# Kernel optimization log

Hardware: AMD Instinct MI355X
Metric: run time of the kernel (lower is better)

Reference implementation:

```python
import jax, jax.numpy as jnp
import numpy as np

B, T, D, H, N, S, FF = 8, 1024, 512, 8, 256, 256, 2048
AUD, TXT = 768, 256  # audio_input_dim, text_feature_dim (hardcoded in module)
EPS = 1e-5


def _ln(x, g, b):
    m = x.mean(-1, keepdims=True)
    v = ((x - m) ** 2).mean(-1, keepdims=True)
    return (x - m) / jnp.sqrt(v + EPS) * g + b


def _lin(x, w, b):
    return x @ w + b


def setup_inputs() -> dict:
    keys = iter(jax.random.split(jax.random.key(0), 64))
    def rn(shape, s=0.02):
        return jax.random.normal(next(keys), shape, jnp.float32) * s
    inp = {
        'x': jax.random.normal(next(keys), (B, T, D), jnp.float32),
        'xf': jax.random.normal(next(keys), (B, AUD), jnp.float32),
        'xw': jax.random.normal(next(keys), (B, N, TXT), jnp.float32),
        'xs': jax.random.normal(next(keys), (B, S, D), jnp.float32),
        # feat_proj (linear variant)
        'fp_w': rn((D, D)), 'fp_b': rn((D,)),
        # self-attention
        'sa_ng': 1.0 + rn((D,)), 'sa_nb': rn((D,)),
        'sa_qw': rn((D, D)), 'sa_qb': rn((D,)),
        'sa_kw': rn((D, D)), 'sa_kb': rn((D,)),
        'sa_vw': rn((D, D)), 'sa_vb': rn((D,)),
        'sa_ow': rn((D, D)), 'sa_ob': rn((D,)),
        # cross-attention
        'ca_ng': 1.0 + rn((D,)), 'ca_nb': rn((D,)),
        'ca_tng': 1.0 + rn((D,)), 'ca_tnb': rn((D,)),
        'ca_sng': 1.0 + rn((D,)), 'ca_snb': rn((D,)),
        'ca_qw': rn((D, D)), 'ca_qb': rn((D,)),
        'ca_kw': rn((D, D)), 'ca_kb': rn((D,)),
        'ca_vw': rn((D, D)), 'ca_vb': rn((D,)),
        'ca_apw': rn((AUD, TXT)), 'ca_apb': rn((TXT,)),
        'ca_atw': rn((TXT, D)), 'ca_atb': rn((D,)),
        'ca_ow': rn((D, D)), 'ca_ob': rn((D,)),
        'an_g': 1.0 + rn((D,)), 'an_b': rn((D,)),
        # FFN
        'ffn_w1': rn((D, FF)), 'ffn_b1': rn((FF,)),
        'ffn_w2': rn((FF, D)), 'ffn_b2': rn((D,)),
        'ffn_ng': 1.0 + rn((D,)), 'ffn_nb': rn((D,)),
        'ffn_ow': rn((D, D)), 'ffn_ob': rn((D,)),
    }
    return inp


def reference(x, xf, xw, xs, fp_w, fp_b, sa_ng, sa_nb, sa_qw, sa_qb, sa_kw, sa_kb,
              sa_vw, sa_vb, sa_ow, sa_ob, ca_ng, ca_nb, ca_tng, ca_tnb, ca_sng, ca_snb,
              ca_qw, ca_qb, ca_kw, ca_kb, ca_vw, ca_vb, ca_apw, ca_apb, ca_atw, ca_atb,
              ca_ow, ca_ob, an_g, an_b, ffn_w1, ffn_b1, ffn_w2, ffn_b2, ffn_ng, ffn_nb,
              ffn_ow, ffn_ob):
    Bx, Tx, Dx = x.shape
    dh = Dx // H
    # feat_proj + detached residual (x_ori = x.detach().clone())
    xp = _lin(x, fp_w, fp_b) + jax.lax.stop_gradient(x)

    # ---- self-attention block ----
    xn = _ln(xp, sa_ng, sa_nb)
    q = _lin(xn, sa_qw, sa_qb).reshape(Bx, Tx, H, dh)
    k = _lin(xn, sa_kw, sa_kb).reshape(Bx, Tx, H, dh)
    v = _lin(xn, sa_vw, sa_vb).reshape(Bx, Tx, H, dh)
    scores = jnp.einsum('bthd,bshd->bths', q, k) / jnp.sqrt(jnp.float32(dh))
    ao = jnp.einsum('bths,bshd->bthd', jax.nn.softmax(scores, -1), v).reshape(Bx, Tx, Dx)
    sa_out = xp + _lin(jax.nn.silu(ao), sa_ow, sa_ob)
    y1 = _ln(sa_out + xp, an_g, an_b)

    # ---- cross-attention block (linear attention over text/audio + semantic) ----
    Nw = xw.shape[1]
    xf_p = _lin(xf, ca_apw, ca_apb)                              # [B, 256]
    xf_e = jnp.broadcast_to(xf_p[:, None, :], (Bx, Nw, TXT))
    xw_xf = _lin(jnp.concatenate([xw, xf_e], axis=1), ca_atw, ca_atb)  # [B, 2N, D]
    tn = _ln(xw_xf, ca_tng, ca_tnb)
    sn = _ln(xs, ca_sng, ca_snb)
    cq = jax.nn.softmax(_lin(_ln(y1, ca_ng, ca_nb), ca_qw, ca_qb).reshape(Bx, Tx, H, dh), -1)
    ck = jax.nn.softmax(_lin(tn, ca_kw, ca_kb).reshape(Bx, 2 * Nw, H, dh), 1)
    sk = jax.nn.softmax(_lin(sn, ca_kw, ca_kb).reshape(Bx, -1, H, dh), 1)
    cv = _lin(tn, ca_vw, ca_vb).reshape(Bx, 2 * Nw, H, dh)
    sv = _lin(sn, ca_vw, ca_vb).reshape(Bx, -1, H, dh)
    att = jnp.einsum('bnhd,bnhl->bhdl', ck, cv)                  # [B,H,dh,dh]
    satt = jnp.einsum('bshd,bshl->bhsl', sk, sv)                 # [B,H,S,dh]
    cy = jnp.einsum('bthd,bhdl->bthl', cq, att).reshape(Bx, Tx, Dx)
    sy = jnp.einsum('bthd,bhsl->bthl', cq, satt).reshape(Bx, Tx, Dx)
    ca_out = y1 + _lin(jax.nn.silu(cy + sy), ca_ow, ca_ob)
    y2 = _ln(ca_out + y1, an_g, an_b)

    # ---- FFN block ----
    h = jax.nn.gelu(_lin(y2, ffn_w1, ffn_b1), approximate=False)
    h = _ln(_lin(h, ffn_w2, ffn_b2), ffn_ng, ffn_nb)
    ffn_out = y2 + _lin(jax.nn.silu(h), ffn_ow, ffn_ob)
    y3 = _ln(ffn_out + y2, an_g, an_b)
    return y3
```

## Files before the change

### kernel.cpp

```cpp
#include <hip/hip_runtime.h>
#include <math.h>

typedef unsigned short u16;
typedef short s16x8 __attribute__((ext_vector_type(8)));
typedef float f32x4 __attribute__((ext_vector_type(4)));
typedef unsigned short u16x8 __attribute__((ext_vector_type(8)));
typedef unsigned short u16x4 __attribute__((ext_vector_type(4)));

#define DD 512

__device__ __forceinline__ float silu_f(float x) { return x / (1.f + __expf(-x)); }
__device__ __forceinline__ float gelu_f(float x) {
  float y = 1.5957691216f * (x + 0.044715f * x * x * x);
  return x / (1.f + __expf(-y));
}
__device__ __forceinline__ u16 f2bf(float f) {
  unsigned u = __float_as_uint(f);
  return (u16)((u + 0x7fffu + ((u >> 16) & 1u)) >> 16);
}
__device__ __forceinline__ float bf2f(u16 u) { return __uint_as_float(((unsigned)u) << 16); }
__device__ __forceinline__ unsigned cvtpk_bf16(float a, float b) {
  unsigned r;
  asm("v_cvt_pk_bf16_f32 %0, %1, %2" : "=v"(r) : "v"(a), "v"(b));
  return r;
}

__device__ __forceinline__ void gload16(const void* g, void* l) {
  __builtin_amdgcn_global_load_lds(
      (const __attribute__((address_space(1))) void*)(g),
      (__attribute__((address_space(3))) void*)(l), 16, 0, 0);
}

template<int ACT, int OB>
__global__ __launch_bounds__(256) void gemm64(
    const u16* __restrict__ A, const u16* __restrict__ Bt,
    const float* __restrict__ bias, const float* __restrict__ res, float res_scale,
    float* __restrict__ outf, float* __restrict__ outf2,
    u16* __restrict__ outb, u16* __restrict__ outb2,
    int M, int N, int K)
{
  __shared__ u16 As[2][4096];
  __shared__ u16 Bs[2][4096];
  const int t = threadIdx.x, l = t & 63, w = t >> 6;
  const int gx = gridDim.x;
  const int nblk = gx * gridDim.y;
  const int id = blockIdx.y * gx + blockIdx.x;
  const int nid = (id & 7) * (nblk >> 3) + (id >> 3);
  const int bm = (nid / gx) << 6, bn = (nid % gx) << 6;
  const int wr = (w >> 1) << 5, wc = (w & 1) << 5;
  f32x4 acc[2][2];
#pragma unroll
  for (int i = 0; i < 2; ++i)
#pragma unroll
    for (int j = 0; j < 2; ++j) acc[i][j] = (f32x4){0.f, 0.f, 0.f, 0.f};

  auto stage = [&](int k0, int buf) {
#pragma unroll
    for (int i = 0; i < 2; ++i) {
      int c = t + (i << 8);
      int row = c >> 3, cq = c & 7;
      int cs = cq ^ (row & 7);
      gload16(A + (size_t)(bm + row) * K + k0 + cs * 8, (char*)As[buf] + (i << 12) + (w << 10));
      gload16(Bt + (size_t)(bn + row) * K + k0 + cs * 8, (char*)Bs[buf] + (i << 12) + (w << 10));
    }
  };
  stage(0, 0);
  asm volatile("s_waitcnt vmcnt(0)" ::: "memory");
  __builtin_amdgcn_s_barrier();

  const int fr = l & 15, q0 = l >> 4;
  const int nk = K >> 6;
  int cur = 0;
  for (int kt = 0; kt < nk; ++kt) {
    if (kt + 1 < nk) stage((kt + 1) << 6, cur ^ 1);
    s16x8 af[2][2], bg[2][2];
#pragma unroll
    for (int kk = 0; kk < 2; ++kk)
#pragma unroll
      for (int i = 0; i < 2; ++i) {
        int ra = wr + i * 16 + fr;
        af[kk][i] = *(const s16x8*)&As[cur][ra * 64 + (((q0 + kk * 4)) ^ (ra & 7)) * 8];
        int rb = wc + i * 16 + fr;
        bg[kk][i] = *(const s16x8*)&Bs[cur][rb * 64 + (((q0 + kk * 4)) ^ (rb & 7)) * 8];
      }
    asm volatile("s_waitcnt lgkmcnt(0)" ::: "memory");
    __builtin_amdgcn_sched_barrier(0);
#pragma unroll
    for (int kk = 0; kk < 2; ++kk)
#pragma unroll
      for (int mi = 0; mi < 2; ++mi)
#pragma unroll
        for (int ni = 0; ni < 2; ++ni)
          acc[mi][ni] = __builtin_amdgcn_mfma_f32_16x16x32_bf16(af[kk][mi], bg[kk][ni], acc[mi][ni], 0, 0, 0);
    asm volatile("s_waitcnt vmcnt(0)" ::: "memory");
    __builtin_amdgcn_s_barrier();
    cur ^= 1;
  }

  const int cr0 = (l >> 4) << 2, cc = l & 15;

  if (OB == 0 || OB == 4) {
    float* fdst = outf;
    int coff = bn, ld = N;
    if (OB == 4) { ld = 512; coff = bn & 511; if (bn >= 512) fdst = outf2; }
#pragma unroll
    for (int ni = 0; ni < 2; ++ni) {
      int n = bn + wc + ni * 16 + cc;
      int col = coff + wc + ni * 16 + cc;
      float bia = bias[n];
#pragma unroll
      for (int mi = 0; mi < 2; ++mi) {
#pragma unroll
        for (int r = 0; r < 4; ++r) {
          int m = bm + wr + mi * 16 + cr0 + r;
          size_t off = (size_t)m * ld + col;
          float o = acc[mi][ni][r] + bia;
          if (ACT == 1) o = gelu_f(o);
          if (res) o = fmaf(res_scale, res[off], o);
          fdst[off] = o;
        }
      }
    }
  } else if (OB == 1 || OB == 5) {
#pragma unroll
    for (int ni = 0; ni < 2; ++ni) {
      int n = bn + wc + ni * 16 + cc;
      float bia = bias[n];
#pragma unroll
      for (int mi = 0; mi < 2; ++mi) {
#pragma unroll
        for (int r = 0; r < 4; ++r) {
          int m = bm + wr + mi * 16 + cr0 + r;
          size_t off = (size_t)m * N + n;
          float o = acc[mi][ni][r] + bia;
          if (ACT == 1) o = gelu_f(o);
          if (OB == 5) o = fmaf(res_scale, res[off], o);
          outb[off] = f2bf(o);
        }
      }
    }
  } else if (OB == 6) {
    float* smem = (float*)&As[0][0];
    float ev[2][2][4];
    float part[2][4];
#pragma unroll
    for (int mi = 0; mi < 2; ++mi)
#pragma unroll
      for (int r = 0; r < 4; ++r) part[mi][r] = 0.f;
#pragma unroll
    for (int ni = 0; ni < 2; ++ni) {
      float bia = bias[bn + wc + ni * 16 + cc];
#pragma unroll
      for (int mi = 0; mi < 2; ++mi)
#pragma unroll
        for (int r = 0; r < 4; ++r) {
          float e = __expf(acc[mi][ni][r] + bia);
          ev[mi][ni][r] = e;
          part[mi][r] += e;
        }
    }
#pragma unroll
    for (int mi = 0; mi < 2; ++mi)
#pragma unroll
      for (int r = 0; r < 4; ++r) {
        float s = part[mi][r];
        s += __shfl_xor(s, 1); s += __shfl_xor(s, 2);
        s += __shfl_xor(s, 4); s += __shfl_xor(s, 8);
        part[mi][r] = s;
      }
    __syncthreads();
#pragma unroll
    for (int mi = 0; mi < 2; ++mi)
#pragma unroll
      for (int r = 0; r < 4; ++r) {
        int trow = wr + mi * 16 + cr0 + r;
        smem[(w & 1) * 64 + trow] = part[mi][r];
      }
    __syncthreads();
#pragma unroll
    for (int mi = 0; mi < 2; ++mi)
#pragma unroll
      for (int r = 0; r < 4; ++r) {
        int trow = wr + mi * 16 + cr0 + r;
        float inv = 1.f / (smem[trow] + smem[64 + trow]);
#pragma unroll
        for (int ni = 0; ni < 2; ++ni) {
          int n = bn + wc + ni * 16 + cc;
          outf[(size_t)(bm + trow) * 512 + n] = ev[mi][ni][r] * inv;
        }
      }
  } else {
    int seg = bn >> 9;
    int colbase = bn & 511;
    if (seg < 2) {
      u16* dst = seg ? outb2 : outb;
#pragma unroll
      for (int ni = 0; ni < 2; ++ni) {
        int col = colbase + wc + ni * 16 + cc;
        float bia = bias[bn + wc + ni * 16 + cc];
#pragma unroll
        for (int mi = 0; mi < 2; ++mi) {
#pragma unroll
          for (int r = 0; r < 4; ++r) {
            int m = bm + wr + mi * 16 + cr0 + r;
            dst[(size_t)m * 512 + col] = f2bf(acc[mi][ni][r] + bia);
          }
        }
      }
    } else {
      u16* tile = &As[0][0];
      __syncthreads();
#pragma unroll
      for (int ni = 0; ni < 2; ++ni) {
        int lc = wc + ni * 16 + cc;
        float bia = bias[bn + wc + ni * 16 + cc];
#pragma unroll
        for (int mi = 0; mi < 2; ++mi) {
          int lm0 = wr + mi * 16 + cr0;
          u16x4 pk;
#pragma unroll
          for (int r = 0; r < 4; ++r) pk[r] = f2bf(acc[mi][ni][r] + bia);
          *(u16x4*)&tile[lc * 64 + (lm0 ^ ((lc & 7) << 3))] = pk;
        }
      }
      __syncthreads();
      int h = colbase >> 6;
      size_t vrow0 = ((size_t)((bm >> 10) * 8 + h)) * 64;
      int d = t >> 3, c8 = (t & 7) << 3;
      *(u16x8*)(((u16*)outf) + (vrow0 + d) * 1024 + (bm & 1023) + c8) =
          *(u16x8*)&tile[d * 64 + (c8 ^ ((d & 7) << 3))];
    }
  }
}

template<int ACT, int OBF>
__global__ __launch_bounds__(512) void gemm8w(
    const u16* __restrict__ A, const u16* __restrict__ Bt,
    const float* __restrict__ bias, float* __restrict__ outf, u16* __restrict__ outb,
    int M, int N, int K)
{
  __shared__ u16 As[2][4096];
  __shared__ u16 Bs[2][8192];
  const int t = threadIdx.x, l = t & 63, w = t >> 6;
  const int gx = gridDim.x;
  const int nblk = gx * gridDim.y;
  const int id = blockIdx.y * gx + blockIdx.x;
  const int nid = (id & 7) * (nblk >> 3) + (id >> 3);
  const int bm = (nid / gx) << 7, bn = (nid % gx) << 8;
  const int wr = (w >> 2) << 6, wc = (w & 3) << 6;
  f32x4 acc[4][4];
#pragma unroll
  for (int i = 0; i < 4; ++i)
#pragma unroll
    for (int j = 0; j < 4; ++j) acc[i][j] = (f32x4){0.f, 0.f, 0.f, 0.f};

  auto stage = [&](int k0, int buf) {
    {
      int row = t >> 2, cq = t & 3;
      int cs = cq ^ ((row >> 1) & 3);
      gload16(A + (size_t)(bm + row) * K + k0 + cs * 8, (char*)As[buf] + (w << 10));
    }
#pragma unroll
    for (int i = 0; i < 2; ++i) {
      int c = t + (i << 9);
      int row = c >> 2, cq = c & 3;
      int cs = cq ^ ((row >> 1) & 3);
      gload16(Bt + (size_t)(bn + row) * K + k0 + cs * 8, (char*)Bs[buf] + ((w + (i << 3)) << 10));
    }
  };
  stage(0, 0);
  asm volatile("s_waitcnt vmcnt(0)" ::: "memory");
  __builtin_amdgcn_s_barrier();

  const int fr = l & 15, q0 = l >> 4;
  const int nk = K >> 5;
  int cur = 0;
  for (int kt = 0; kt < nk; ++kt) {
    if (kt + 1 < nk) stage((kt + 1) << 5, cur ^ 1);
    s16x8 af[4], bg[4];
#pragma unroll
    for (int i = 0; i < 4; ++i) {
      int ra = wr + i * 16 + fr;
      af[i] = *(const s16x8*)&As[cur][ra * 32 + (q0 ^ ((ra >> 1) & 3)) * 8];
      int rb = wc + i * 16 + fr;
      bg[i] = *(const s16x8*)&Bs[cur][rb * 32 + (q0 ^ ((rb >> 1) & 3)) * 8];
    }
    asm volatile("s_waitcnt lgkmcnt(0)" ::: "memory");
    __builtin_amdgcn_sched_barrier(0);
#pragma unroll
    for (int mi = 0; mi < 4; ++mi)
#pragma unroll
      for (int ni = 0; ni < 4; ++ni)
        acc[mi][ni] = __builtin_amdgcn_mfma_f32_16x16x32_bf16(af[mi], bg[ni], acc[mi][ni], 0, 0, 0);
    asm volatile("s_waitcnt vmcnt(0)" ::: "memory");
    __builtin_amdgcn_s_barrier();
    cur ^= 1;
  }

  const int cr0 = (l >> 4) << 2, cc = l & 15;
#pragma unroll
  for (int ni = 0; ni < 4; ++ni) {
    int n = bn + wc + ni * 16 + cc;
    float bia = bias[n];
#pragma unroll
    for (int mi = 0; mi < 4; ++mi) {
#pragma unroll
      for (int r = 0; r < 4; ++r) {
        int m = bm + wr + mi * 16 + cr0 + r;
        size_t off = (size_t)m * N + n;
        float o = acc[mi][ni][r] + bia;
        if (ACT == 1) o = gelu_f(o);
        if (OBF) outb[off] = f2bf(o);
        else outf[off] = o;
      }
    }
  }
}

__global__ __launch_bounds__(256) void xfp_k(
    const float* __restrict__ xf, const u16* __restrict__ apwT,
    const float* __restrict__ bias, float* __restrict__ xfp)
{
  int wid = blockIdx.x * 4 + (threadIdx.x >> 6);
  int lane = threadIdx.x & 63;
  int b = wid >> 8, n = wid & 255;
  const u16* wp = apwT + (size_t)n * 768;
  const float* xp = xf + (size_t)b * 768;
  float s = 0.f;
#pragma unroll
  for (int j = 0; j < 12; ++j) s = fmaf(xp[lane + j * 64], bf2f(wp[lane + j * 64]), s);
#pragma unroll
  for (int m = 1; m < 64; m <<= 1) s += __shfl_xor(s, m);
  if (lane == 0) xfp[wid] = s + bias[n];
}

__global__ __launch_bounds__(256) void biascat_k(
    const float* __restrict__ qb, const float* __restrict__ kb, const float* __restrict__ vb,
    const float* __restrict__ ckb, const float* __restrict__ cvb,
    float* __restrict__ bQKV, float* __restrict__ bKV)
{
  int t = blockIdx.x * 256 + threadIdx.x;
  if (t < 512) bQKV[t] = qb[t];
  else if (t < 1024) bQKV[t] = kb[t - 512];
  else if (t < 1536) bQKV[t] = vb[t - 1024];
  else if (t < 2048) bKV[t - 1536] = ckb[t - 1536];
  else if (t < 2560) bKV[t - 1536] = cvb[t - 2048];
}

__global__ __launch_bounds__(256) void ln_k(
    const float* __restrict__ src, const float* __restrict__ g,
    const float* __restrict__ b, float* __restrict__ out32, u16* __restrict__ out16,
    int rows, int do_silu)
{
  int lane = threadIdx.x & 63, wv = threadIdx.x >> 6;
  int row = (blockIdx.x << 2) + wv;
  if (row >= rows) return;
  const float* p = src + (size_t)row * DD;
  float4 v0 = *(const float4*)(p + lane * 4);
  float4 v1 = *(const float4*)(p + 256 + lane * 4);
  float s = v0.x + v0.y + v0.z + v0.w + v1.x + v1.y + v1.z + v1.w;
  float ss = v0.x*v0.x + v0.y*v0.y + v0.z*v0.z + v0.w*v0.w
           + v1.x*v1.x + v1.y*v1.y + v1.z*v1.z + v1.w*v1.w;
#pragma unroll
  for (int m = 1; m < 64; m <<= 1) { s += __shfl_xor(s, m); ss += __shfl_xor(ss, m); }
  float mean = s * (1.f / 512.f);
  float var = ss * (1.f / 512.f) - mean * mean;
  float rstd = rsqrtf(var + 1e-5f);
  float4 g0 = *(const float4*)(g + lane * 4);
  float4 g1 = *(const float4*)(g + 256 + lane * 4);
  float4 b0 = *(const float4*)(b + lane * 4);
  float4 b1 = *(const float4*)(b + 256 + lane * 4);
  float o[8];
  o[0] = (v0.x - mean) * rstd * g0.x + b0.x;
  o[1] = (v0.y - mean) * rstd * g0.y + b0.y;
  o[2] = (v0.z - mean) * rstd * g0.z + b0.z;
  o[3] = (v0.w - mean) * rstd * g0.w + b0.w;
  o[4] = (v1.x - mean) * rstd * g1.x + b1.x;
  o[5] = (v1.y - mean) * rstd * g1.y + b1.y;
  o[6] = (v1.z - mean) * rstd * g1.z + b1.z;
  o[7] = (v1.w - mean) * rstd * g1.w + b1.w;
  if (do_silu) {
#pragma unroll
    for (int j = 0; j < 8; ++j) o[j] = silu_f(o[j]);
  }
  if (out32) {
    *(float4*)(out32 + (size_t)row * DD + lane * 4) = make_float4(o[0], o[1], o[2], o[3]);
    *(float4*)(out32 + (size_t)row * DD + 256 + lane * 4) = make_float4(o[4], o[5], o[6], o[7]);
  }
  if (out16) {
    u16x4 h0, h1;
#pragma unroll
    for (int j = 0; j < 4; ++j) { h0[j] = f2bf(o[j]); h1[j] = f2bf(o[4 + j]); }
    *(u16x4*)(out16 + (size_t)row * DD + lane * 4) = h0;
    *(u16x4*)(out16 + (size_t)row * DD + 256 + lane * 4) = h1;
  }
}

__global__ __launch_bounds__(256) void lnb_k(
    const u16* __restrict__ src, const float* __restrict__ g,
    const float* __restrict__ b, float* __restrict__ out32, u16* __restrict__ out16,
    int rows, int do_silu)
{
  int lane = threadIdx.x & 63, wv = threadIdx.x >> 6;
  int row = (blockIdx.x << 2) + wv;
  if (row >= rows) return;
  const u16* p = src + (size_t)row * DD;
  u16x4 a0 = *(const u16x4*)(p + lane * 4);
  u16x4 a1 = *(const u16x4*)(p + 256 + lane * 4);
  float v[8];
#pragma unroll
  for (int j = 0; j < 4; ++j) { v[j] = bf2f(a0[j]); v[4 + j] = bf2f(a1[j]); }
  float s = 0.f, ss = 0.f;
#pragma unroll
  for (int j = 0; j < 8; ++j) { s += v[j]; ss = fmaf(v[j], v[j], ss); }
#pragma unroll
  for (int m = 1; m < 64; m <<= 1) { s += __shfl_xor(s, m); ss += __shfl_xor(ss, m); }
  float mean = s * (1.f / 512.f);
  float var = ss * (1.f / 512.f) - mean * mean;
  float rstd = rsqrtf(var + 1e-5f);
  float4 g0 = *(const float4*)(g + lane * 4);
  float4 g1 = *(const float4*)(g + 256 + lane * 4);
  float4 b0 = *(const float4*)(b + lane * 4);
  float4 b1 = *(const float4*)(b + 256 + lane * 4);
  float o[8];
  o[0] = (v[0] - mean) * rstd * g0.x + b0.x;
  o[1] = (v[1] - mean) * rstd * g0.y + b0.y;
  o[2] = (v[2] - mean) * rstd * g0.z + b0.z;
  o[3] = (v[3] - mean) * rstd * g0.w + b0.w;
  o[4] = (v[4] - mean) * rstd * g1.x + b1.x;
  o[5] = (v[5] - mean) * rstd * g1.y + b1.y;
  o[6] = (v[6] - mean) * rstd * g1.z + b1.z;
  o[7] = (v[7] - mean) * rstd * g1.w + b1.w;
  if (do_silu) {
#pragma unroll
    for (int j = 0; j < 8; ++j) o[j] = silu_f(o[j]);
  }
  if (out32) {
    *(float4*)(out32 + (size_t)row * DD + lane * 4) = make_float4(o[0], o[1], o[2], o[3]);
    *(float4*)(out32 + (size_t)row * DD + 256 + lane * 4) = make_float4(o[4], o[5], o[6], o[7]);
  }
  if (out16) {
    u16x4 h0, h1;
#pragma unroll
    for (int j = 0; j < 4; ++j) { h0[j] = f2bf(o[j]); h1[j] = f2bf(o[4 + j]); }
    *(u16x4*)(out16 + (size_t)row * DD + lane * 4) = h0;
    *(u16x4*)(out16 + (size_t)row * DD + 256 + lane * 4) = h1;
  }
}

__global__ __launch_bounds__(256) void ln2_k(
    const u16* __restrict__ src, const float* __restrict__ g1, const float* __restrict__ b1,
    const float* __restrict__ g2, const float* __restrict__ b2,
    float* __restrict__ out1, u16* __restrict__ out2, int rows)
{
  int lane = threadIdx.x & 63, wv = threadIdx.x >> 6;
  int row = (blockIdx.x << 2) + wv;
  if (row >= rows) return;
  const u16* p = src + (size_t)row * DD;
  u16x4 a0 = *(const u16x4*)(p + lane * 4);
  u16x4 a1 = *(const u16x4*)(p + 256 + lane * 4);
  float v[8];
#pragma unroll
  for (int j = 0; j < 4; ++j) { v[j] = bf2f(a0[j]); v[4 + j] = bf2f(a1[j]); }
  float s = 0.f, ss = 0.f;
#pragma unroll
  for (int j = 0; j < 8; ++j) { s += v[j]; ss = fmaf(v[j], v[j], ss); }
#pragma unroll
  for (int m = 1; m < 64; m <<= 1) { s += __shfl_xor(s, m); ss += __shfl_xor(ss, m); }
  float mean = s * (1.f / 512.f);
  float rstd = rsqrtf(ss * (1.f / 512.f) - mean * mean + 1e-5f);
  float4 G0 = *(const float4*)(g1 + lane * 4);
  float4 G1 = *(const float4*)(g1 + 256 + lane * 4);
  float4 B0 = *(const float4*)(b1 + lane * 4);
  float4 B1 = *(const float4*)(b1 + 256 + lane * 4);
  float y[8];
  y[0] = (v[0] - mean) * rstd * G0.x + B0.x;
  y[1] = (v[1] - mean) * rstd * G0.y + B0.y;
  y[2] = (v[2] - mean) * rstd * G0.z + B0.z;
  y[3] = (v[3] - mean) * rstd * G0.w + B0.w;
  y[4] = (v[4] - mean) * rstd * G1.x + B1.x;
  y[5] = (v[5] - mean) * rstd * G1.y + B1.y;
  y[6] = (v[6] - mean) * rstd * G1.z + B1.z;
  y[7] = (v[7] - mean) * rstd * G1.w + B1.w;
  *(float4*)(out1 + (size_t)row * DD + lane * 4) = make_float4(y[0], y[1], y[2], y[3]);
  *(float4*)(out1 + (size_t)row * DD + 256 + lane * 4) = make_float4(y[4], y[5], y[6], y[7]);
  float s2 = 0.f, ss2 = 0.f;
#pragma unroll
  for (int j = 0; j < 8; ++j) { s2 += y[j]; ss2 = fmaf(y[j], y[j], ss2); }
#pragma unroll
  for (int m = 1; m < 64; m <<= 1) { s2 += __shfl_xor(s2, m); ss2 += __shfl_xor(ss2, m); }
  float m2 = s2 * (1.f / 512.f);
  float r2 = rsqrtf(ss2 * (1.f / 512.f) - m2 * m2 + 1e-5f);
  float4 H0 = *(const float4*)(g2 + lane * 4);
  float4 H1 = *(const float4*)(g2 + 256 + lane * 4);
  float4 C0 = *(const float4*)(b2 + lane * 4);
  float4 C1 = *(const float4*)(b2 + 256 + lane * 4);
  u16x4 h0, h1;
  h0[0] = f2bf((y[0] - m2) * r2 * H0.x + C0.x);
  h0[1] = f2bf((y[1] - m2) * r2 * H0.y + C0.y);
  h0[2] = f2bf((y[2] - m2) * r2 * H0.z + C0.z);
  h0[3] = f2bf((y[3] - m2) * r2 * H0.w + C0.w);
  h1[0] = f2bf((y[4] - m2) * r2 * H1.x + C1.x);
  h1[1] = f2bf((y[5] - m2) * r2 * H1.y + C1.y);
  h1[2] = f2bf((y[6] - m2) * r2 * H1.z + C1.z);
  h1[3] = f2bf((y[7] - m2) * r2 * H1.w + C1.w);
  *(u16x4*)(out2 + (size_t)row * DD + lane * 4) = h0;
  *(u16x4*)(out2 + (size_t)row * DD + 256 + lane * 4) = h1;
}

__global__ __launch_bounds__(256) void attn3_k(
    const u16* __restrict__ q, const u16* __restrict__ k,
    const u16* __restrict__ vt, u16* __restrict__ out)
{
  __shared__ __align__(16) char KVb[2][2][8192];
  __shared__ __align__(16) char QP[16384];
  __shared__ float Lr[4][32];

  const int t = threadIdx.x, l = t & 63, w = t >> 6;
  const int id = blockIdx.x;
  const int blk = (id & 7) * 64 + (id >> 3);
  const int qt = blk & 7, h = (blk >> 3) & 7, b = blk >> 6;
  const size_t qbase = ((size_t)(b * 1024 + qt * 128)) * 512 + h * 64;
  const size_t kbase = ((size_t)(b * 1024)) * 512 + h * 64;
  const size_t vbase = ((size_t)((b * 8 + h) * 64)) * 1024;

#pragma unroll
  for (int i = 0; i < 4; ++i) {
    int chunk = i * 256 + w * 64 + l;
    int row = chunk >> 3, c = chunk & 7;
    int cs = c ^ (row & 7);
    gload16(q + qbase + (size_t)row * 512 + cs * 8, QP + (i * 256 + w * 64) * 16);
  }
  auto stageKV = [&](int st, int buf) {
#pragma unroll
    for (int i = 0; i < 2; ++i) {
      int chunk = i * 256 + w * 64 + l;
      int row = chunk >> 3, c = chunk & 7;
      int cs = c ^ (row & 7);
      gload16(k + kbase + (size_t)(st * 64 + row) * 512 + cs * 8,
              KVb[buf][0] + (i * 256 + w * 64) * 16);
      gload16(vt + vbase + (size_t)row * 1024 + st * 64 + cs * 8,
              KVb[buf][1] + (i * 256 + w * 64) * 16);
    }
  };
  stageKV(0, 0);
  __syncthreads();

  s16x8 qf[2][2];
#pragma unroll
  for (int ti = 0; ti < 2; ++ti)
#pragma unroll
    for (int kk = 0; kk < 2; ++kk) {
      int row = w * 32 + ti * 16 + (l & 15);
      int ch = ((l >> 4) + kk * 4) ^ (row & 7);
      qf[ti][kk] = *(const s16x8*)(QP + row * 128 + ch * 16);
    }

  f32x4 oacc[2][4];
#pragma unroll
  for (int qi = 0; qi < 2; ++qi)
#pragma unroll
    for (int dj = 0; dj < 4; ++dj) oacc[qi][dj] = (f32x4){0.f, 0.f, 0.f, 0.f};
  float lsum[2] = {0.f, 0.f};

  int cur = 0;
  for (int st = 0; st < 16; ++st) {
    if (st + 1 < 16) stageKV(st + 1, cur ^ 1);
    f32x4 sacc[4][2];
#pragma unroll
    for (int si = 0; si < 4; ++si)
#pragma unroll
      for (int ti = 0; ti < 2; ++ti) sacc[si][ti] = (f32x4){0.f, 0.f, 0.f, 0.f};
#pragma unroll
    for (int si = 0; si < 4; ++si) {
#pragma unroll
      for (int kk = 0; kk < 2; ++kk) {
        int s = si * 16 + (l & 15);
        int ch = ((l >> 4) + kk * 4) ^ (s & 7);
        s16x8 kf = *(const s16x8*)(KVb[cur][0] + s * 128 + ch * 16);
#pragma unroll
        for (int ti = 0; ti < 2; ++ti)
          sacc[si][ti] = __builtin_amdgcn_mfma_f32_16x16x32_bf16(kf, qf[ti][kk], sacc[si][ti], 0, 0, 0);
      }
    }
#pragma unroll
    for (int si = 0; si < 4; ++si)
#pragma unroll
      for (int ti = 0; ti < 2; ++ti) {
        float e0 = __expf(sacc[si][ti][0] * 0.125f);
        float e1 = __expf(sacc[si][ti][1] * 0.125f);
        float e2 = __expf(sacc[si][ti][2] * 0.125f);
        float e3 = __expf(sacc[si][ti][3] * 0.125f);
        lsum[ti] += (e0 + e1) + (e2 + e3);
        uint2 pk2;
        pk2.x = cvtpk_bf16(e0, e1);
        pk2.y = cvtpk_bf16(e2, e3);
        int tl = ti * 16 + (l & 15);
        int sb = (si * 16 + (l >> 4) * 4) * 2;
        *(uint2*)(QP + w * 4096 + tl * 128 + (sb ^ ((tl & 7) << 4))) = pk2;
      }
#pragma unroll
    for (int kk = 0; kk < 2; ++kk) {
      s16x8 pf[2];
#pragma unroll
      for (int qi = 0; qi < 2; ++qi) {
        int tl = qi * 16 + (l & 15);
        int ch = ((l >> 4) + kk * 4) ^ (tl & 7);
        pf[qi] = *(const s16x8*)(QP + w * 4096 + tl * 128 + ch * 16);
      }
#pragma unroll
      for (int dj = 0; dj < 4; ++dj) {
        int d = dj * 16 + (l & 15);
        int ch = ((l >> 4) + kk * 4) ^ (d & 7);
        s16x8 vf = *(const s16x8*)(KVb[cur][1] + d * 128 + ch * 16);
#pragma unroll
        for (int qi = 0; qi < 2; ++qi)
          oacc[qi][dj] = __builtin_amdgcn_mfma_f32_16x16x32_bf16(pf[qi], vf, oacc[qi][dj], 0, 0, 0);
      }
    }
    cur ^= 1;
    __syncthreads();
  }

#pragma unroll
  for (int ti = 0; ti < 2; ++ti) {
    lsum[ti] += __shfl_xor(lsum[ti], 16);
    lsum[ti] += __shfl_xor(lsum[ti], 32);
    Lr[w][ti * 16 + (l & 15)] = lsum[ti];
  }
  __syncthreads();
  u16* otile = (u16*)QP;
#pragma unroll
  for (int qi = 0; qi < 2; ++qi) {
    float linv[4];
#pragma unroll
    for (int r = 0; r < 4; ++r) linv[r] = 1.f / Lr[w][qi * 16 + (l >> 4) * 4 + r];
#pragma unroll
    for (int dj = 0; dj < 4; ++dj) {
#pragma unroll
      for (int r = 0; r < 4; ++r) {
        int trl = w * 32 + qi * 16 + (l >> 4) * 4 + r;
        otile[trl * 64 + dj * 16 + (l & 15)] = f2bf(silu_f(oacc[qi][dj][r] * linv[r]));
      }
    }
  }
  __syncthreads();
#pragma unroll
  for (int p = 0; p < 4; ++p) {
    int flat = p * 256 + t;
    int row = flat >> 3, c8 = (flat & 7) << 3;
    *(u16x8*)(out + ((size_t)(b * 1024 + qt * 128 + row)) * 512 + h * 64 + c8) =
        *(u16x8*)&otile[row * 64 + c8];
  }
}

template<int NL>
__global__ __launch_bounds__(256) void smseq_k(float* __restrict__ p)
{
  __shared__ float red[256];
  int t = threadIdx.x;
  int ci = t & 15, nj = t >> 4;
  int b = blockIdx.x >> 5, cg = blockIdx.x & 31;
  int col = cg * 16 + ci;
  float vals[NL / 16];
  float s = 0.f;
#pragma unroll
  for (int j = 0; j < NL / 16; ++j) {
    float x = __expf(p[((size_t)(b * NL) + nj + j * 16) * 512 + col]);
    vals[j] = x; s += x;
  }
  red[t] = s;
  __syncthreads();
  float tot = 0.f;
#pragma unroll
  for (int j = 0; j < 16; ++j) tot += red[ci + j * 16];
  float inv = 1.f / tot;
#pragma unroll
  for (int j = 0; j < NL / 16; ++j)
    p[((size_t)(b * NL) + nj + j * 16) * 512 + col] = vals[j] * inv;
}

__global__ __launch_bounds__(256) void build_xc_k(
    const float* __restrict__ xw, const float* __restrict__ xfp, u16* __restrict__ xc)
{
  int idx = blockIdx.x * 256 + threadIdx.x;
  int c = idx & 255, n = (idx >> 8) & 511, b = idx >> 17;
  float val = (n < 256) ? xw[((b << 8) + n) * 256 + c] : xfp[(b << 8) + c];
  xc[idx] = f2bf(val);
}

__global__ __launch_bounds__(256) void attmat1_k(
    const float* __restrict__ ckp, const float* __restrict__ cvp, float* __restrict__ attp)
{
  __shared__ float a_s[64][68];
  __shared__ float b_s[64][68];
  int bh = blockIdx.x >> 3, sl = blockIdx.x & 7;
  int h = bh & 7, b = bh >> 3;
  int n0 = sl << 6;
  int tid = threadIdx.x;
  int d = tid & 63, lg = tid >> 6;
  float acc[16];
#pragma unroll
  for (int j = 0; j < 16; ++j) acc[j] = 0.f;
#pragma unroll
  for (int i = 0; i < 4; ++i) {
    int f = tid + (i << 8);
    int row = f >> 4, c4 = (f & 15) << 2;
    size_t src = ((size_t)(b * 512 + n0 + row)) * DD + h * 64 + c4;
    *(float4*)&a_s[row][c4] = *(const float4*)(ckp + src);
    *(float4*)&b_s[row][c4] = *(const float4*)(cvp + src);
  }
  __syncthreads();
  for (int nn = 0; nn < 64; ++nn) {
    float av = a_s[nn][d];
#pragma unroll
    for (int j4 = 0; j4 < 4; ++j4) {
      float4 b4 = *(float4*)&b_s[nn][lg * 16 + j4 * 4];
      acc[j4*4+0] = fmaf(av, b4.x, acc[j4*4+0]);
      acc[j4*4+1] = fmaf(av, b4.y, acc[j4*4+1]);
      acc[j4*4+2] = fmaf(av, b4.z, acc[j4*4+2]);
      acc[j4*4+3] = fmaf(av, b4.w, acc[j4*4+3]);
    }
  }
  float* op = attp + ((size_t)(bh * 8 + sl)) * 4096 + d * 64 + lg * 16;
#pragma unroll
  for (int j4 = 0; j4 < 4; ++j4)
    *(float4*)(op + j4 * 4) = make_float4(acc[j4*4+0], acc[j4*4+1], acc[j4*4+2], acc[j4*4+3]);
}

__global__ __launch_bounds__(256) void attred_k(
    const float* __restrict__ attp, float* __restrict__ att)
{
  int idx = (blockIdx.x * 256 + threadIdx.x) * 4;
  int bh = idx >> 12, e = idx & 4095;
  float4 s = make_float4(0.f, 0.f, 0.f, 0.f);
#pragma unroll
  for (int sl = 0; sl < 8; ++sl) {
    float4 v = *(const float4*)&attp[((size_t)(bh * 8 + sl)) * 4096 + e];
    s.x += v.x; s.y += v.y; s.z += v.z; s.w += v.w;
  }
  *(float4*)&att[idx] = s;
}

__global__ __launch_bounds__(256) void rowsum64_k(
    const float* __restrict__ skp, float* __restrict__ r)
{
  int wv = threadIdx.x >> 6, l = threadIdx.x & 63;
  int g16 = l >> 4, l16 = l & 15;
  for (int it = 0; it < 16; ++it) {
    int rid = blockIdx.x * 256 + wv * 64 + it * 4 + g16;
    const float* base = skp + (size_t)(rid >> 3) * 512 + (rid & 7) * 64;
    float4 v = *(const float4*)(base + l16 * 4);
    float s = (v.x + v.y) + (v.z + v.w);
    s += __shfl_xor(s, 1); s += __shfl_xor(s, 2);
    s += __shfl_xor(s, 4); s += __shfl_xor(s, 8);
    if (l16 == 0) r[rid] = s;
  }
}

__global__ __launch_bounds__(256) void sy2_k(
    const float* __restrict__ r, const float* __restrict__ svp, float* __restrict__ sy)
{
  __shared__ float part[4][64];
  int b = blockIdx.x >> 3, h = blockIdx.x & 7;
  int t = threadIdx.x;
  int li = t & 63, sg = t >> 6;
  float acc = 0.f;
  for (int j = 0; j < 64; ++j) {
    int s = sg * 64 + j;
    size_t ix = (size_t)(b * 256 + s);
    acc = fmaf(r[ix * 8 + h], svp[ix * 512 + h * 64 + li], acc);
  }
  part[sg][li] = acc;
  __syncthreads();
  if (t < 64) sy[(b * 8 + h) * 64 + t] = (part[0][t] + part[1][t]) + (part[2][t] + part[3][t]);
}

__global__ __launch_bounds__(256) void cy_k(
    const float* __restrict__ cq, const float* __restrict__ att,
    const float* __restrict__ sy, u16* __restrict__ out)
{
  __shared__ float atts[64][68];
  __shared__ float qs[64][68];
  __shared__ float sys[64];
  int blk = blockIdx.x;
  int tt = blk & 15, h = (blk >> 4) & 7, b = blk >> 7;
  int t0 = tt << 6;
  int tid = threadIdx.x;
#pragma unroll
  for (int i = 0; i < 4; ++i) {
    int f = tid + (i << 8);
    int row = f >> 4, c4 = (f & 15) << 2;
    *(float4*)&atts[row][c4] = *(const float4*)(att + (size_t)(b * 8 + h) * 4096 + row * 64 + c4);
    *(float4*)&qs[row][c4] = *(const float4*)(cq + ((size_t)(b * 1024 + t0 + row)) * DD + h * 64 + c4);
  }
  if (tid < 64) sys[tid] = sy[(b * 8 + h) * 64 + tid];
  __syncthreads();
  int r = tid >> 2, lg = tid & 3;
  float acc[16];
#pragma unroll
  for (int j = 0; j < 16; ++j) acc[j] = 0.f;
  for (int d = 0; d < 64; ++d) {
    float qv = qs[r][d];
#pragma unroll
    for (int j4 = 0; j4 < 4; ++j4) {
      float4 a4 = *(float4*)&atts[d][lg * 16 + j4 * 4];
      acc[j4*4+0] = fmaf(qv, a4.x, acc[j4*4+0]);
      acc[j4*4+1] = fmaf(qv, a4.y, acc[j4*4+1]);
      acc[j4*4+2] = fmaf(qv, a4.z, acc[j4*4+2]);
      acc[j4*4+3] = fmaf(qv, a4.w, acc[j4*4+3]);
    }
  }
  u16* op = out + ((size_t)(b * 1024 + t0 + r)) * DD + h * 64 + lg * 16;
#pragma unroll
  for (int j4 = 0; j4 < 4; ++j4) {
    u16x4 o4;
    o4[0] = f2bf(silu_f(acc[j4*4+0] + sys[lg * 16 + j4*4+0]));
    o4[1] = f2bf(silu_f(acc[j4*4+1] + sys[lg * 16 + j4*4+1]));
    o4[2] = f2bf(silu_f(acc[j4*4+2] + sys[lg * 16 + j4*4+2]));
    o4[3] = f2bf(silu_f(acc[j4*4+3] + sys[lg * 16 + j4*4+3]));
    *(u16x4*)(op + j4 * 4) = o4;
  }
}

__global__ __launch_bounds__(256) void cvtf2b_k(const float* __restrict__ in, u16* __restrict__ out, int n)
{
  int i = (blockIdx.x * 256 + threadIdx.x) * 4;
  if (i >= n) return;
  float4 v = *(const float4*)(in + i);
  u16x4 o;
  o[0] = f2bf(v.x); o[1] = f2bf(v.y); o[2] = f2bf(v.z); o[3] = f2bf(v.w);
  *(u16x4*)(out + i) = o;
}

__global__ __launch_bounds__(256) void wtrans_k(const float* __restrict__ W, u16* __restrict__ Wt, int Kd, int Nd)
{
  __shared__ float tile[32][33];
  int ntn = Nd >> 5;
  int tk = blockIdx.x / ntn, tn = blockIdx.x % ntn;
  int lx = threadIdx.x & 31, ly = threadIdx.x >> 5;
#pragma unroll
  for (int i = 0; i < 4; ++i)
    tile[ly + 8 * i][lx] = W[(size_t)(tk * 32 + ly + 8 * i) * Nd + tn * 32 + lx];
  __syncthreads();
#pragma unroll
  for (int i = 0; i < 4; ++i)
    Wt[(size_t)(tn * 32 + ly + 8 * i) * Kd + tk * 32 + lx] = f2bf(tile[lx][ly + 8 * i]);
}

struct W10 { const float* w[10]; u16* o[10]; };
__global__ __launch_bounds__(256) void wtrans10_k(W10 p)
{
  __shared__ float tile[32][33];
  int wi = blockIdx.x >> 8;
  int tb = blockIdx.x & 255;
  int tk = tb >> 4, tn = tb & 15;
  const float* W = p.w[wi];
  u16* Wt = p.o[wi];
  int lx = threadIdx.x & 31, ly = threadIdx.x >> 5;
#pragma unroll
  for (int i = 0; i < 4; ++i)
    tile[ly + 8 * i][lx] = W[(size_t)(tk * 32 + ly + 8 * i) * 512 + tn * 32 + lx];
  __syncthreads();
#pragma unroll
  for (int i = 0; i < 4; ++i)
    Wt[(size_t)(tn * 32 + ly + 8 * i) * 512 + tk * 32 + lx] = f2bf(tile[lx][ly + 8 * i]);
}

extern "C" void kernel_launch(void* const* d_in, const int* in_sizes, int n_in,
                              void* d_out, int out_size, void* d_ws, size_t ws_size,
                              hipStream_t stream)
{
  const float* x      = (const float*)d_in[0];
  const float* xf     = (const float*)d_in[1];
  const float* xw     = (const float*)d_in[2];
  const float* xs     = (const float*)d_in[3];
  const float* fp_w   = (const float*)d_in[4];
  const float* fp_b   = (const float*)d_in[5];
  const float* sa_ng  = (const float*)d_in[6];
  const float* sa_nb  = (const float*)d_in[7];
  const float* sa_qw  = (const float*)d_in[8];
  const float* sa_qb  = (const float*)d_in[9];
  const float* sa_kw  = (const float*)d_in[10];
  const float* sa_kb  = (const float*)d_in[11];
  const float* sa_vw  = (const float*)d_in[12];
  const float* sa_vb  = (const float*)d_in[13];
  const float* sa_ow  = (const float*)d_in[14];
  const float* sa_ob  = (const float*)d_in[15];
  const float* ca_ng  = (const float*)d_in[16];
  const float* ca_nb  = (const float*)d_in[17];
  const float* ca_tng = (const float*)d_in[18];
  const float* ca_tnb = (const float*)d_in[19];
  const float* ca_sng = (const float*)d_in[20];
  const float* ca_snb = (const float*)d_in[21];
  const float* ca_qw  = (const float*)d_in[22];
  const float* ca_qb  = (const float*)d_in[23];
  const float* ca_kw  = (const float*)d_in[24];
  const float* ca_kb  = (const float*)d_in[25];
  const float* ca_vw  = (const float*)d_in[26];
  const float* ca_vb  = (const float*)d_in[27];
  const float* ca_apw = (const float*)d_in[28];
  const float* ca_apb = (const float*)d_in[29];
  const float* ca_atw = (const float*)d_in[30];
  const float* ca_atb = (const float*)d_in[31];
  const float* ca_ow  = (const float*)d_in[32];
  const float* ca_ob  = (const float*)d_in[33];
  const float* an_g   = (const float*)d_in[34];
  const float* an_b   = (const float*)d_in[35];
  const float* ffn_w1 = (const float*)d_in[36];
  const float* ffn_b1 = (const float*)d_in[37];
  const float* ffn_w2 = (const float*)d_in[38];
  const float* ffn_b2 = (const float*)d_in[39];
  const float* ffn_ng = (const float*)d_in[40];
  const float* ffn_nb = (const float*)d_in[41];
  const float* ffn_ow = (const float*)d_in[42];
  const float* ffn_ob = (const float*)d_in[43];

  float* ws = (float*)d_ws;
  float* slotZ = ws;
  float* slotP = ws + 4194304;
  u16* Zb = (u16*)slotZ;
  u16* S1 = (u16*)(ws + 8388608);
  u16* S2 = (u16*)(ws + 10485760);
  u16* S3 = (u16*)(ws + 12582912);
  u16* S4 = (u16*)(ws + 14680064);
  u16* Vt = (u16*)(ws + 16777216);
  u16* S6 = (u16*)(ws + 18874368);
  float* ck  = ws + 20971520;
  float* sk  = ws + 23068672;
  float* cv  = ws + 24117248;
  float* sv  = ws + 26214400;
  float* tnr = ws + 27262976;
  u16* tn = (u16*)(ws + 29360128);
  u16* sn = (u16*)(ws + 30408704);
  u16* h1 = (u16*)(ws + 20971520);
  u16* xc = (u16*)(ws + 30932992);
  float* att = ws + 31457280;
  float* xfp = ws + 31719424;
  float* sy  = ws + 31723520;
  u16* wb = (u16*)(ws + 31727616);
  u16* fp_wt   = wb;
  u16* sa_qwt  = wb + 262144;
  u16* sa_kwt  = wb + 524288;
  u16* sa_vwt  = wb + 786432;
  u16* sa_owt  = wb + 1048576;
  u16* ca_qwt  = wb + 1310720;
  u16* ca_kwt  = wb + 1572864;
  u16* ca_vwt  = wb + 1835008;
  u16* ca_owt  = wb + 2097152;
  u16* ffn_owt = wb + 2359296;
  u16* ca_atwt = wb + 2621440;
  u16* ffn_w1t = wb + 2752512;
  u16* ffn_w2t = wb + 3801088;
  u16* apwT    = wb + 4849664;
  float* bQKV  = (float*)(wb + 5046272);
  float* bKV   = bQKV + 1536;
  float* attp  = ws + 34260992;
  float* rws   = ws + 36358144;

  dim3 blk(256);
  auto g64 = [](int M, int N) { return dim3((unsigned)(N >> 6), (unsigned)(M >> 6)); };

  cvtf2b_k<<<dim3(4096), blk, 0, stream>>>(x, S1, 4194304);
  W10 wp;
  wp.w[0] = fp_w;  wp.o[0] = fp_wt;
  wp.w[1] = sa_qw; wp.o[1] = sa_qwt;
  wp.w[2] = sa_kw; wp.o[2] = sa_kwt;
  wp.w[3] = sa_vw; wp.o[3] = sa_vwt;
  wp.w[4] = sa_ow; wp.o[4] = sa_owt;
  wp.w[5] = ca_qw; wp.o[5] = ca_qwt;
  wp.w[6] = ca_kw; wp.o[6] = ca_kwt;
  wp.w[7] = ca_vw; wp.o[7] = ca_vwt;
  wp.w[8] = ca_ow; wp.o[8] = ca_owt;
  wp.w[9] = ffn_ow; wp.o[9] = ffn_owt;
  wtrans10_k<<<dim3(2560), blk, 0, stream>>>(wp);
  wtrans_k<<<dim3(128), blk, 0, stream>>>(ca_atw, ca_atwt, 256, 512);
  wtrans_k<<<dim3(1024), blk, 0, stream>>>(ffn_w1, ffn_w1t, 512, 2048);
  wtrans_k<<<dim3(1024), blk, 0, stream>>>(ffn_w2, ffn_w2t, 2048, 512);
  wtrans_k<<<dim3(192), blk, 0, stream>>>(ca_apw, apwT, 768, 256);
  biascat_k<<<dim3(10), blk, 0, stream>>>(sa_qb, sa_kb, sa_vb, ca_kb, ca_vb, bQKV, bKV);

  xfp_k<<<dim3(512), blk, 0, stream>>>(xf, apwT, ca_apb, xfp);
  build_xc_k<<<dim3(4096), blk, 0, stream>>>(xw, xfp, xc);
  gemm64<0,0><<<g64(4096, 512), blk, 0, stream>>>(xc, ca_atwt, ca_atb, nullptr, 0.f, tnr, nullptr, nullptr, nullptr, 4096, 512, 256);
  ln_k<<<dim3(1024), blk, 0, stream>>>(tnr, ca_tng, ca_tnb, nullptr, tn, 4096, 0);
  ln_k<<<dim3(512), blk, 0, stream>>>(xs, ca_sng, ca_snb, nullptr, sn, 2048, 0);

  gemm64<0,0><<<g64(8192, 512), blk, 0, stream>>>(S1, fp_wt, fp_b, x, 1.f, slotP, nullptr, nullptr, nullptr, 8192, 512, 512);
  ln_k<<<dim3(2048), blk, 0, stream>>>(slotP, sa_ng, sa_nb, nullptr, S2, 8192, 0);
  gemm64<0,3><<<g64(8192, 1536), blk, 0, stream>>>(S2, sa_qwt, bQKV, nullptr, 0.f, (float*)Vt, nullptr, S3, S4, 8192, 1536, 512);
  attn3_k<<<dim3(512), blk, 0, stream>>>(S3, S4, Vt, S6);
  gemm64<0,5><<<g64(8192, 512), blk, 0, stream>>>(S6, sa_owt, sa_ob, slotP, 2.f, nullptr, nullptr, Zb, nullptr, 8192, 512, 512);
  ln2_k<<<dim3(2048), blk, 0, stream>>>(Zb, an_g, an_b, ca_ng, ca_nb, slotP, S1, 8192);

  gemm64<0,6><<<g64(8192, 512), blk, 0, stream>>>(S1, ca_qwt, ca_qb, nullptr, 0.f, slotZ, nullptr, nullptr, nullptr, 8192, 512, 512);
  gemm64<0,4><<<g64(6144, 1024), blk, 0, stream>>>(tn, ca_kwt, bKV, nullptr, 0.f, ck, cv, nullptr, nullptr, 6144, 1024, 512);
  smseq_k<512><<<dim3(256), blk, 0, stream>>>(ck);
  smseq_k<256><<<dim3(256), blk, 0, stream>>>(sk);
  attmat1_k<<<dim3(512), blk, 0, stream>>>(ck, cv, attp);
  attred_k<<<dim3(256), blk, 0, stream>>>(attp, att);
  rowsum64_k<<<dim3(64), blk, 0, stream>>>(sk, rws);
  sy2_k<<<dim3(64), blk, 0, stream>>>(rws, sv, sy);
  cy_k<<<dim3(1024), blk, 0, stream>>>(slotZ, att, sy, S2);
  gemm64<0,5><<<g64(8192, 512), blk, 0, stream>>>(S2, ca_owt, ca_ob, slotP, 2.f, nullptr, nullptr, Zb, nullptr, 8192, 512, 512);
  lnb_k<<<dim3(2048), blk, 0, stream>>>(Zb, an_g, an_b, slotP, S3, 8192, 0);

  gemm8w<1,1><<<dim3(8, 64), dim3(512), 0, stream>>>(S3, ffn_w1t, ffn_b1, nullptr, h1, 8192, 2048, 512);
  gemm64<0,1><<<g64(8192, 512), blk, 0, stream>>>(h1, ffn_w2t, ffn_b2, nullptr, 0.f, nullptr, nullptr, Zb, nullptr, 8192, 512, 2048);
  lnb_k<<<dim3(2048), blk, 0, stream>>>(Zb, ffn_ng, ffn_nb, nullptr, S1, 8192, 1);
  gemm64<0,5><<<g64(8192, 512), blk, 0, stream>>>(S1, ffn_owt, ffn_ob, slotP, 2.f, nullptr, nullptr, Zb, nullptr, 8192, 512, 512);
  lnb_k<<<dim3(2048), blk, 0, stream>>>(Zb, an_g, an_b, (float*)d_out, nullptr, 8192, 0);
}
```

Measured before the change: 330.0 us.

## Merge small kernels and store cross-attention query softmax as bf16

Cuts launch count by merging the four weight-transpose launches into one table-driven kernel, the two sequence-softmax launches into one, and the rowsum and sy launches into a single kernel that keeps row sums in shared memory. The softmaxed cross-attention query is now written as bf16 into the Zb buffer instead of fp32, roughly halving that 8192x512 store and the cy_k read. The trade is lower precision on the query softmax and loss of compile-time unrolling in the softmax loops, which now use runtime trip counts with a fixed-size register array.

```diff
diff --git a/kernel.cpp b/kernel.cpp
--- a/kernel.cpp
+++ b/kernel.cpp
@@ -186,7 +186,7 @@
 #pragma unroll
         for (int ni = 0; ni < 2; ++ni) {
           int n = bn + wc + ni * 16 + cc;
-          outf[(size_t)(bm + trow) * 512 + n] = ev[mi][ni][r] * inv;
+          outb[(size_t)(bm + trow) * 512 + n] = f2bf(ev[mi][ni][r] * inv);
         }
       }
   } else {
@@ -654,30 +654,39 @@
   }
 }
 
-template<int NL>
-__global__ __launch_bounds__(256) void smseq_k(float* __restrict__ p)
+__device__ __forceinline__ void smseq_body(float* p, int b, int cg, int NL, int nj, int ci, float* red, int t)
+{
+  int col = cg * 16 + ci;
+  float vals[32];
+  float s = 0.f;
+  int nit = NL / 16;
+  for (int j = 0; j < nit; ++j) {
+    float x = __expf(p[((size_t)(b * NL) + nj + j * 16) * 512 + col]);
+    vals[j] = x; s += x;
+  }
+  red[t] = s;
+  __syncthreads();
+  float tot = 0.f;
+#pragma unroll
+  for (int j = 0; j < 16; ++j) tot += red[ci + j * 16];
+  float inv = 1.f / tot;
+  for (int j = 0; j < nit; ++j)
+    p[((size_t)(b * NL) + nj + j * 16) * 512 + col] = vals[j] * inv;
+}
+
+__global__ __launch_bounds__(256) void smseq2_k(float* __restrict__ ck, float* __restrict__ sk)
 {
   __shared__ float red[256];
   int t = threadIdx.x;
   int ci = t & 15, nj = t >> 4;
-  int b = blockIdx.x >> 5, cg = blockIdx.x & 31;
-  int col = cg * 16 + ci;
-  float vals[NL / 16];
-  float s = 0.f;
-#pragma unroll
-  for (int j = 0; j < NL / 16; ++j) {
-    float x = __expf(p[((size_t)(b * NL) + nj + j * 16) * 512 + col]);
-    vals[j] = x; s += x;
-  }
-  red[t] = s;
-  __syncthreads();
-  float tot = 0.f;
-#pragma unroll
-  for (int j = 0; j < 16; ++j) tot += red[ci + j * 16];
-  float inv = 1.f / tot;
-#pragma unroll
-  for (int j = 0; j < NL / 16; ++j)
-    p[((size_t)(b * NL) + nj + j * 16) * 512 + col] = vals[j] * inv;
+  if (blockIdx.x < 256) {
+    int b = blockIdx.x >> 5, cg = blockIdx.x & 31;
+    smseq_body(ck, b, cg, 512, nj, ci, red, t);
+  } else {
+    int blk = blockIdx.x - 256;
+    int b = blk >> 5, cg = blk & 31;
+    smseq_body(sk, b, cg, 256, nj, ci, red, t);
+  }
 }
 
 __global__ __launch_bounds__(256) void build_xc_k(
@@ -742,34 +751,30 @@
   *(float4*)&att[idx] = s;
 }
 
-__global__ __launch_bounds__(256) void rowsum64_k(
-    const float* __restrict__ skp, float* __restrict__ r)
-{
-  int wv = threadIdx.x >> 6, l = threadIdx.x & 63;
-  int g16 = l >> 4, l16 = l & 15;
-  for (int it = 0; it < 16; ++it) {
-    int rid = blockIdx.x * 256 + wv * 64 + it * 4 + g16;
-    const float* base = skp + (size_t)(rid >> 3) * 512 + (rid & 7) * 64;
-    float4 v = *(const float4*)(base + l16 * 4);
-    float s = (v.x + v.y) + (v.z + v.w);
-    s += __shfl_xor(s, 1); s += __shfl_xor(s, 2);
-    s += __shfl_xor(s, 4); s += __shfl_xor(s, 8);
-    if (l16 == 0) r[rid] = s;
-  }
-}
-
-__global__ __launch_bounds__(256) void sy2_k(
-    const float* __restrict__ r, const float* __restrict__ svp, float* __restrict__ sy)
-{
+__global__ __launch_bounds__(256) void sy3_k(
+    const float* __restrict__ skp, const float* __restrict__ svp, float* __restrict__ sy)
+{
+  __shared__ float rsum[256];
   __shared__ float part[4][64];
   int b = blockIdx.x >> 3, h = blockIdx.x & 7;
   int t = threadIdx.x;
+  int g16 = t >> 4, l16 = t & 15;
+  for (int it = 0; it < 16; ++it) {
+    int s = g16 * 16 + it;
+    const float* base = skp + ((size_t)(b * 256 + s)) * 512 + h * 64;
+    float4 v = *(const float4*)(base + l16 * 4);
+    float sm = (v.x + v.y) + (v.z + v.w);
+    sm += __shfl_xor(sm, 1); sm += __shfl_xor(sm, 2);
+    sm += __shfl_xor(sm, 4); sm += __shfl_xor(sm, 8);
+    if (l16 == 0) rsum[s] = sm;
+  }
+  __syncthreads();
   int li = t & 63, sg = t >> 6;
   float acc = 0.f;
   for (int j = 0; j < 64; ++j) {
     int s = sg * 64 + j;
     size_t ix = (size_t)(b * 256 + s);
-    acc = fmaf(r[ix * 8 + h], svp[ix * 512 + h * 64 + li], acc);
+    acc = fmaf(rsum[s], svp[ix * 512 + h * 64 + li], acc);
   }
   part[sg][li] = acc;
   __syncthreads();
@@ -777,7 +782,7 @@
 }
 
 __global__ __launch_bounds__(256) void cy_k(
-    const float* __restrict__ cq, const float* __restrict__ att,
+    const u16* __restrict__ cq, const float* __restrict__ att,
     const float* __restrict__ sy, u16* __restrict__ out)
 {
   __shared__ float atts[64][68];
@@ -792,7 +797,11 @@
     int f = tid + (i << 8);
     int row = f >> 4, c4 = (f & 15) << 2;
     *(float4*)&atts[row][c4] = *(const float4*)(att + (size_t)(b * 8 + h) * 4096 + row * 64 + c4);
-    *(float4*)&qs[row][c4] = *(const float4*)(cq + ((size_t)(b * 1024 + t0 + row)) * DD + h * 64 + c4);
+    u16x4 qv4 = *(const u16x4*)(cq + ((size_t)(b * 1024 + t0 + row)) * DD + h * 64 + c4);
+    qs[row][c4 + 0] = bf2f(qv4[0]);
+    qs[row][c4 + 1] = bf2f(qv4[1]);
+    qs[row][c4 + 2] = bf2f(qv4[2]);
+    qs[row][c4 + 3] = bf2f(qv4[3]);
   }
   if (tid < 64) sys[tid] = sy[(b * 8 + h) * 64 + tid];
   __syncthreads();
@@ -833,21 +842,6 @@
   *(u16x4*)(out + i) = o;
 }
 
-__global__ __launch_bounds__(256) void wtrans_k(const float* __restrict__ W, u16* __restrict__ Wt, int Kd, int Nd)
-{
-  __shared__ float tile[32][33];
-  int ntn = Nd >> 5;
-  int tk = blockIdx.x / ntn, tn = blockIdx.x % ntn;
-  int lx = threadIdx.x & 31, ly = threadIdx.x >> 5;
-#pragma unroll
-  for (int i = 0; i < 4; ++i)
-    tile[ly + 8 * i][lx] = W[(size_t)(tk * 32 + ly + 8 * i) * Nd + tn * 32 + lx];
-  __syncthreads();
-#pragma unroll
-  for (int i = 0; i < 4; ++i)
-    Wt[(size_t)(tn * 32 + ly + 8 * i) * Kd + tk * 32 + lx] = f2bf(tile[lx][ly + 8 * i]);
-}
-
 struct W10 { const float* w[10]; u16* o[10]; };
 __global__ __launch_bounds__(256) void wtrans10_k(W10 p)
 {
@@ -865,6 +859,31 @@
 #pragma unroll
   for (int i = 0; i < 4; ++i)
     Wt[(size_t)(tn * 32 + ly + 8 * i) * 512 + tk * 32 + lx] = f2bf(tile[lx][ly + 8 * i]);
+}
+
+struct WT4 { const float* w[4]; u16* o[4]; int kd[4]; int nd[4]; int base[4]; };
+__global__ __launch_bounds__(256) void wtrans4_k(WT4 p)
+{
+  __shared__ float tile[32][33];
+  int blk = blockIdx.x;
+  int e = 3;
+  if (blk < p.base[1]) e = 0;
+  else if (blk < p.base[2]) e = 1;
+  else if (blk < p.base[3]) e = 2;
+  int idx = blk - p.base[e];
+  const float* W = p.w[e];
+  u16* Wt = p.o[e];
+  int Kd = p.kd[e], Nd = p.nd[e];
+  int ntn = Nd >> 5;
+  int tk = idx / ntn, tn = idx % ntn;
+  int lx = threadIdx.x & 31, ly = threadIdx.x >> 5;
+#pragma unroll
+  for (int i = 0; i < 4; ++i)
+    tile[ly + 8 * i][lx] = W[(size_t)(tk * 32 + ly + 8 * i) * Nd + tn * 32 + lx];
+  __syncthreads();
+#pragma unroll
+  for (int i = 0; i < 4; ++i)
+    Wt[(size_t)(tn * 32 + ly + 8 * i) * Kd + tk * 32 + lx] = f2bf(tile[lx][ly + 8 * i]);
 }
 
 extern "C" void kernel_launch(void* const* d_in, const int* in_sizes, int n_in,
@@ -956,7 +975,6 @@
   float* bQKV  = (float*)(wb + 5046272);
   float* bKV   = bQKV + 1536;
   float* attp  = ws + 34260992;
-  float* rws   = ws + 36358144;
 
   dim3 blk(256);
   auto g64 = [](int M, int N) { return dim3((unsigned)(N >> 6), (unsigned)(M >> 6)); };
@@ -974,10 +992,12 @@
   wp.w[8] = ca_ow; wp.o[8] = ca_owt;
   wp.w[9] = ffn_ow; wp.o[9] = ffn_owt;
   wtrans10_k<<<dim3(2560), blk, 0, stream>>>(wp);
-  wtrans_k<<<dim3(128), blk, 0, stream>>>(ca_atw, ca_atwt, 256, 512);
-  wtrans_k<<<dim3(1024), blk, 0, stream>>>(ffn_w1, ffn_w1t, 512, 2048);
-  wtrans_k<<<dim3(1024), blk, 0, stream>>>(ffn_w2, ffn_w2t, 2048, 512);
-  wtrans_k<<<dim3(192), blk, 0, stream>>>(ca_apw, apwT, 768, 256);
+  WT4 wq;
+  wq.w[0] = ca_atw; wq.o[0] = ca_atwt; wq.kd[0] = 256;  wq.nd[0] = 512;  wq.base[0] = 0;
+  wq.w[1] = ffn_w1; wq.o[1] = ffn_w1t; wq.kd[1] = 512;  wq.nd[1] = 2048; wq.base[1] = 128;
+  wq.w[2] = ffn_w2; wq.o[2] = ffn_w2t; wq.kd[2] = 2048; wq.nd[2] = 512;  wq.base[2] = 1152;
+  wq.w[3] = ca_apw; wq.o[3] = apwT;    wq.kd[3] = 768;  wq.nd[3] = 256;  wq.base[3] = 2176;
+  wtrans4_k<<<dim3(2368), blk, 0, stream>>>(wq);
   biascat_k<<<dim3(10), blk, 0, stream>>>(sa_qb, sa_kb, sa_vb, ca_kb, ca_vb, bQKV, bKV);
 
   xfp_k<<<dim3(512), blk, 0, stream>>>(xf, apwT, ca_apb, xfp);
@@ -993,15 +1013,13 @@
   gemm64<0,5><<<g64(8192, 512), blk, 0, stream>>>(S6, sa_owt, sa_ob, slotP, 2.f, nullptr, nullptr, Zb, nullptr, 8192, 512, 512);
   ln2_k<<<dim3(2048), blk, 0, stream>>>(Zb, an_g, an_b, ca_ng, ca_nb, slotP, S1, 8192);
 
-  gemm64<0,6><<<g64(8192, 512), blk, 0, stream>>>(S1, ca_qwt, ca_qb, nullptr, 0.f, slotZ, nullptr, nullptr, nullptr, 8192, 512, 512);
+  gemm64<0,6><<<g64(8192, 512), blk, 0, stream>>>(S1, ca_qwt, ca_qb, nullptr, 0.f, nullptr, nullptr, Zb, nullptr, 8192, 512, 512);
   gemm64<0,4><<<g64(6144, 1024), blk, 0, stream>>>(tn, ca_kwt, bKV, nullptr, 0.f, ck, cv, nullptr, nullptr, 6144, 1024, 512);
-  smseq_k<512><<<dim3(256), blk, 0, stream>>>(ck);
-  smseq_k<256><<<dim3(256), blk, 0, stream>>>(sk);
+  smseq2_k<<<dim3(512), blk, 0, stream>>>(ck, sk);
   attmat1_k<<<dim3(512), blk, 0, stream>>>(ck, cv, attp);
   attred_k<<<dim3(256), blk, 0, stream>>>(attp, att);
-  rowsum64_k<<<dim3(64), blk, 0, stream>>>(sk, rws);
-  sy2_k<<<dim3(64), blk, 0, stream>>>(rws, sv, sy);
-  cy_k<<<dim3(1024), blk, 0, stream>>>(slotZ, att, sy, S2);
+  sy3_k<<<dim3(64), blk, 0, stream>>>(sk, sv, sy);
+  cy_k<<<dim3(1024), blk, 0, stream>>>(Zb, att, sy, S2);
   gemm64<0,5><<<g64(8192, 512), blk, 0, stream>>>(S2, ca_owt, ca_ob, slotP, 2.f, nullptr, nullptr, Zb, nullptr, 8192, 512, 512);
   lnb_k<<<dim3(2048), blk, 0, stream>>>(Zb, an_g, an_b, slotP, S3, 8192, 0);
 
```

Result: no change. 330.6 us, median of 2 (+0.2%).
